# Optimization experiments

Hardware: AMD Instinct MI355X
Metric: run time of the kernel (lower is better)

The kernel has to match this reference:

```python
import jax, jax.numpy as jnp
import numpy as np

N_NODES = 50000
N_EDGES = 800000
IN_C = 128
OUT_C = 128
ALPHA = 0.2  # leaky_relu negative slope (args.egat_alpha)
EDGE_K = 3   # edgefeat width, fixed by W_out in-dim = 3*out_channels


def setup_inputs() -> dict:
    key = jax.random.key(0)
    k = jax.random.split(key, 7)
    h = jax.random.normal(k[0], (N_NODES, IN_C), dtype=jnp.float32)
    edge_index = jax.random.randint(k[1], (2, N_EDGES), 0, N_NODES, dtype=jnp.int64)
    edgefeat = jax.random.uniform(k[2], (N_EDGES, EDGE_K), dtype=jnp.float32)
    # glorot-initialized linear weights (stored as [in, out] for x @ W)
    def glorot(kk, fan_in, fan_out):
        lim = jnp.sqrt(6.0 / (fan_in + fan_out)).astype(jnp.float32)
        return jax.random.uniform(kk, (fan_in, fan_out), jnp.float32, -lim, lim)
    W = glorot(k[3], IN_C, OUT_C)
    a1 = glorot(k[4], OUT_C, 1)
    a2 = glorot(k[5], OUT_C, 1)
    W_out = glorot(k[6], EDGE_K * OUT_C, OUT_C)
    return {"h": h, "edge_index": edge_index, "edgefeat": edgefeat,
            "W": W, "a1": a1, "a2": a2, "W_out": W_out}


def reference(h, edge_index, edgefeat, W, a1, a2, W_out):
    src = edge_index[0]  # j: message source
    dst = edge_index[1]  # i: aggregation target
    n = h.shape[0]

    Wh = h @ W                                   # [N, C]
    s1 = Wh @ a1                                 # [N, 1] alpha_j scores
    s2 = Wh @ a2                                 # [N, 1] alpha_i scores

    # edge_update: leaky_relu(alpha_j + alpha_i) * edge_attr, then edge softmax over dst
    e = s1[src] + s2[dst]                        # [E, 1]
    e = jnp.where(e >= 0, e, ALPHA * e)
    alpha = e * edgefeat                         # [E, 3]
    m = jax.ops.segment_max(alpha, dst, num_segments=n)      # [N, 3]
    m = jnp.where(jnp.isfinite(m), m, 0.0)
    ex = jnp.exp(alpha - m[dst])
    denom = jax.ops.segment_sum(ex, dst, num_segments=n)     # [N, 3]
    att = ex / (denom[dst] + 1e-16)              # [E, 3] (dropout p applied at eval -> identity)

    # message: outer product att[E,3] x x_j[E,C] -> [E, 3C] -> W_out -> [E, C]
    x_j = Wh[src]                                # [E, C]
    msg = (att[:, :, None] * x_j[:, None, :]).reshape(att.shape[0], EDGE_K * Wh.shape[1])
    msg = msg @ W_out                            # [E, C]

    # aggregate: sum at destination nodes
    out = jax.ops.segment_sum(msg, dst, num_segments=n)      # [N, C]
    return out
```

## Files before the change

kernel.cpp:

```cpp
#include <hip/hip_runtime.h>
#include <hip/hip_bf16.h>

#define ALPHA 0.2f
typedef unsigned int uint32;
typedef __attribute__((ext_vector_type(8))) short short8;
typedef __attribute__((ext_vector_type(4))) float f32x4;

static __device__ __forceinline__ unsigned short f2bf(float f) {
    unsigned int u = __float_as_uint(f);
    u += 0x7fffu + ((u >> 16) & 1u);
    return (unsigned short)(u >> 16);
}
static __device__ __forceinline__ uint32 pk2bf(float lo, float hi) {
    return (uint32)f2bf(lo) | ((uint32)f2bf(hi) << 16);
}
static __device__ __forceinline__ float bflo(uint32 u) { return __uint_as_float(u << 16); }
static __device__ __forceinline__ float bfhi(uint32 u) { return __uint_as_float(u & 0xffff0000u); }

__global__ __launch_bounds__(256) void k1_hist_prep(const int* __restrict__ ei,
                                                    int* __restrict__ counts,
                                                    int* __restrict__ eslot, int E,
                                                    const float* __restrict__ W,
                                                    const float* __restrict__ Wout,
                                                    const float* __restrict__ a1,
                                                    const float* __restrict__ a2,
                                                    unsigned short* __restrict__ WBT,
                                                    unsigned short* __restrict__ WoutT,
                                                    float* __restrict__ w1f,
                                                    float* __restrict__ w2f, int nbh) {
    const int tid = threadIdx.x;
    if ((int)blockIdx.x < nbh) {
        int e = blockIdx.x * 256 + tid;
        if (e < E) eslot[e] = atomicAdd(&counts[ei[E + e]], 1);
        return;
    }
    int bp = blockIdx.x - nbh;
    if (bp < 8) {
        for (int n = bp * 16; n < bp * 16 + 16; ++n)
            for (int c = tid; c < 128; c += 256)
                WBT[n * 128 + c] = f2bf(W[c * 128 + n]);
    } else if (bp < 24) {
        int q = bp - 8;
        for (int n = q * 8; n < q * 8 + 8; ++n)
            for (int c = tid; c < 384; c += 256)
                WoutT[n * 384 + c] = f2bf(Wout[c * 128 + n]);
    } else {
        if (tid < 128) {
            float acc1 = 0.f, acc2 = 0.f;
            for (int c = 0; c < 128; ++c) {
                float w = W[tid * 128 + c];
                acc1 += w * a1[c];
                acc2 += w * a2[c];
            }
            w1f[tid] = acc1;
            w2f[tid] = acc2;
        }
    }
}

__global__ __launch_bounds__(256) void k2_mmy_scan(const float* __restrict__ h,
                                                   const unsigned short* __restrict__ WBT,
                                                   const float* __restrict__ w1f,
                                                   const float* __restrict__ w2f,
                                                   unsigned short* __restrict__ Whb,
                                                   float* __restrict__ s1,
                                                   uint2* __restrict__ PR, int M,
                                                   const int* __restrict__ counts,
                                                   int* __restrict__ rowptr,
                                                   int N, int E, int nbm) {
    __shared__ unsigned short As[64 * 128];
    __shared__ unsigned short Bs[128 * 128];
    __shared__ float ws1[128], ws2[128];
    __shared__ int wsums[4];
    __shared__ int base_s;
    const int tid = threadIdx.x;

    if ((int)blockIdx.x >= nbm) {
        const int bs   = blockIdx.x - nbm;
        const int lane = tid & 63, wv = tid >> 6;
        const int limit = bs * 1024;
        int acc = 0;
        for (int i = tid * 4; i < limit; i += 1024) {
            int4 v = *(const int4*)(counts + i);
            acc += v.x + v.y + v.z + v.w;
        }
#pragma unroll
        for (int off = 32; off > 0; off >>= 1) acc += __shfl_down(acc, off);
        if (lane == 0) wsums[wv] = acc;
        __syncthreads();
        if (tid == 0) base_s = wsums[0] + wsums[1] + wsums[2] + wsums[3];
        __syncthreads();
        int i0 = bs * 1024 + tid * 4;
        int v0 = 0, v1 = 0, v2 = 0, v3 = 0;
        if (i0 + 3 < N) {
            int4 v = *(const int4*)(counts + i0);
            v0 = v.x; v1 = v.y; v2 = v.z; v3 = v.w;
        } else {
            if (i0 + 0 < N) v0 = counts[i0 + 0];
            if (i0 + 1 < N) v1 = counts[i0 + 1];
            if (i0 + 2 < N) v2 = counts[i0 + 2];
            if (i0 + 3 < N) v3 = counts[i0 + 3];
        }
        int tt = v0 + v1 + v2 + v3;
        int incl = tt;
#pragma unroll
        for (int off = 1; off < 64; off <<= 1) {
            int t = __shfl_up(incl, off);
            if (lane >= off) incl += t;
        }
        __syncthreads();
        if (lane == 63) wsums[wv] = incl;
        __syncthreads();
        int woff = 0;
        for (int w2 = 0; w2 < wv; ++w2) woff += wsums[w2];
        int base = base_s + woff + (incl - tt);
        if (i0 + 0 < N) { rowptr[i0 + 0] = base;                PR[i0 + 0].y = (uint32)base; }
        if (i0 + 1 < N) { rowptr[i0 + 1] = base + v0;           PR[i0 + 1].y = (uint32)(base + v0); }
        if (i0 + 2 < N) { rowptr[i0 + 2] = base + v0 + v1;      PR[i0 + 2].y = (uint32)(base + v0 + v1); }
        if (i0 + 3 < N) { rowptr[i0 + 3] = base + v0 + v1 + v2; PR[i0 + 3].y = (uint32)(base + v0 + v1 + v2); }
        if (bs == 0 && tid == 0) rowptr[N] = E;
        return;
    }

    const int lane = tid & 63;
    const int w    = tid >> 6;
    const int row0 = blockIdx.x * 64;

    if (tid < 128) ws1[tid] = w1f[tid];
    else           ws2[tid - 128] = w2f[tid - 128];
    __syncthreads();

    const float4* h4 = (const float4*)h;
    float sp1[4], sp2[4];
#pragma unroll
    for (int m = 0; m < 4; ++m) { sp1[m] = 0.f; sp2[m] = 0.f; }
#pragma unroll
    for (int m = 0; m < 4; ++m) {
        int i = m * 256 + tid;
        int r = i >> 4, g = i & 15;
        int rg = row0 + r;
        float4 va = make_float4(0.f, 0.f, 0.f, 0.f), vb = va;
        if (rg < M) {
            va = h4[(size_t)rg * 32 + g * 2];
            vb = h4[(size_t)rg * 32 + g * 2 + 1];
        }
        float4 wa1 = *(const float4*)(ws1 + g * 8);
        float4 wb1 = *(const float4*)(ws1 + g * 8 + 4);
        float4 wa2 = *(const float4*)(ws2 + g * 8);
        float4 wb2 = *(const float4*)(ws2 + g * 8 + 4);
        sp1[m] += va.x * wa1.x + va.y * wa1.y + va.z * wa1.z + va.w * wa1.w
                + vb.x * wb1.x + vb.y * wb1.y + vb.z * wb1.z + vb.w * wb1.w;
        sp2[m] += va.x * wa2.x + va.y * wa2.y + va.z * wa2.z + va.w * wa2.w
                + vb.x * wb2.x + vb.y * wb2.y + vb.z * wb2.z + vb.w * wb2.w;
        uint4 u;
        u.x = pk2bf(va.x, va.y); u.y = pk2bf(va.z, va.w);
        u.z = pk2bf(vb.x, vb.y); u.w = pk2bf(vb.z, vb.w);
        *(uint4*)(As + r * 128 + ((g ^ (r & 15)) * 8)) = u;
    }
#pragma unroll
    for (int m = 0; m < 4; ++m) {
#pragma unroll
        for (int off = 1; off < 16; off <<= 1) {
            sp1[m] += __shfl_xor(sp1[m], off);
            sp2[m] += __shfl_xor(sp2[m], off);
        }
    }
    if ((tid & 15) == 0) {
#pragma unroll
        for (int m = 0; m < 4; ++m) {
            int rg = row0 + m * 16 + (tid >> 4);
            if (rg < M) { s1[rg] = sp1[m]; PR[rg].x = __float_as_uint(sp2[m]); }
        }
    }

#pragma unroll
    for (int m = 0; m < 8; ++m) {
        int i = m * 256 + tid;
        int n = i >> 4, g = i & 15;
        uint4 v = *(const uint4*)(WBT + n * 128 + g * 8);
        *(uint4*)(Bs + n * 128 + ((g ^ (n & 15)) * 8)) = v;
    }
    __syncthreads();

    const int ml   = lane & 15;
    const int quad = lane >> 4;
    f32x4 acc[8];
#pragma unroll
    for (int nt = 0; nt < 8; ++nt) acc[nt] = (f32x4){0.f, 0.f, 0.f, 0.f};
#pragma unroll
    for (int kc = 0; kc < 4; ++kc) {
        int gl = ((kc * 4 + quad) ^ ml) * 8;
        short8 af = *(const short8*)(As + (w * 16 + ml) * 128 + gl);
#pragma unroll
        for (int nt = 0; nt < 8; ++nt) {
            short8 bf = *(const short8*)(Bs + (nt * 16 + ml) * 128 + gl);
            acc[nt] = __builtin_amdgcn_mfma_f32_16x16x32_bf16(af, bf, acc[nt], 0, 0, 0);
        }
    }
    __syncthreads();
    unsigned short* Ct = Bs;
    int lrow = w * 16 + quad * 4;
#pragma unroll
    for (int r = 0; r < 4; ++r)
#pragma unroll
        for (int nt = 0; nt < 8; ++nt)
            Ct[(lrow + r) * 136 + nt * 16 + ml] = f2bf(acc[nt][r]);
    __syncthreads();
#pragma unroll
    for (int m = 0; m < 4; ++m) {
        int i = m * 256 + tid;
        int r2 = i >> 4, g = i & 15;
        int rg = row0 + r2;
        uint4 v = *(const uint4*)(Ct + r2 * 136 + g * 8);
        if (rg < M)
            *(uint4*)(Whb + (size_t)rg * 128 + g * 8) = v;
    }
}

__global__ __launch_bounds__(256) void scatter_kernel(const int* __restrict__ ei,
                                                      const float* __restrict__ ef,
                                                      const float* __restrict__ s1,
                                                      const uint2* __restrict__ PR,
                                                      const int* __restrict__ eslot,
                                                      uint2* __restrict__ rec8, int E) {
    int e = blockIdx.x * blockDim.x + threadIdx.x;
    if (e >= E) return;
    int src = ei[e];
    int dst = ei[E + e];
    uint2 pr = PR[dst];
    float s = s1[src] + __uint_as_float(pr.x);
    s = (s >= 0.f) ? s : ALPHA * s;
    unsigned short b0 = f2bf(__expf(s * ef[e * 3 + 0]));
    unsigned short b1 = f2bf(__expf(s * ef[e * 3 + 1]));
    unsigned short b2 = f2bf(__expf(s * ef[e * 3 + 2]));
    uint2 rv;
    rv.x = (uint32)src | ((uint32)(b0 & 0x7fffu) << 17);
    rv.y = (uint32)(b1 & 0x7fffu) | ((uint32)(b2 & 0x7fffu) << 15);
    int pos = (int)pr.y + eslot[e];
    rec8[pos] = rv;
}

__global__ __launch_bounds__(256) void agg_fused(const uint2* __restrict__ rec8,
                                                 const int* __restrict__ rowptr,
                                                 const uint32* __restrict__ Yu,
                                                 const unsigned short* __restrict__ WoutT,
                                                 float* __restrict__ out, int N) {
    __shared__ uint32 zs32[16 * 192];
    const int tid  = threadIdx.x;
    const int lane = tid & 63, w = tid >> 6;
    const int ml   = lane & 15, quad = lane >> 4;
    const int nb   = blockIdx.x * 16;

#pragma unroll
    for (int rnd = 0; rnd < 4; ++rnd) {
        int r    = rnd * 4 + w;
        int node = nb + r;
        if (node >= N) continue;
        int beg = rowptr[node], end = rowptr[node + 1];

        float d0 = 0.f, d1 = 0.f, d2 = 0.f;
        float z0l = 0.f, z0h = 0.f, z1l = 0.f, z1h = 0.f, z2l = 0.f, z2h = 0.f;
        int j = beg;
        for (; j + 7 < end; j += 8) {
            uint2 rr[8];
#pragma unroll
            for (int q = 0; q < 8; ++q) rr[q] = rec8[j + q];
            uint32 sx[8], sy[8];
#pragma unroll
            for (int q = 0; q < 8; ++q) {
                sx[q] = __builtin_amdgcn_readfirstlane(rr[q].x);
                sy[q] = __builtin_amdgcn_readfirstlane(rr[q].y);
            }
            uint32 u[8];
#pragma unroll
            for (int q = 0; q < 8; ++q)
                u[q] = Yu[(size_t)(sx[q] & 0x1ffffu) * 64 + lane];
#pragma unroll
            for (int q = 0; q < 8; ++q) {
                float w0 = __uint_as_float((sx[q] >> 1) & 0x7fff0000u);
                float w1 = __uint_as_float((sy[q] << 16) & 0x7fff0000u);
                float w2 = __uint_as_float((sy[q] << 1) & 0x7fff0000u);
                d0 += w0; d1 += w1; d2 += w2;
                float yl = bflo(u[q]), yh = bfhi(u[q]);
                z0l += w0 * yl; z0h += w0 * yh;
                z1l += w1 * yl; z1h += w1 * yh;
                z2l += w2 * yl; z2h += w2 * yh;
            }
        }
        for (; j + 3 < end; j += 4) {
            uint2 rr[4];
#pragma unroll
            for (int q = 0; q < 4; ++q) rr[q] = rec8[j + q];
            uint32 sx[4], sy[4];
#pragma unroll
            for (int q = 0; q < 4; ++q) {
                sx[q] = __builtin_amdgcn_readfirstlane(rr[q].x);
                sy[q] = __builtin_amdgcn_readfirstlane(rr[q].y);
            }
            uint32 u[4];
#pragma unroll
            for (int q = 0; q < 4; ++q)
                u[q] = Yu[(size_t)(sx[q] & 0x1ffffu) * 64 + lane];
#pragma unroll
            for (int q = 0; q < 4; ++q) {
                float w0 = __uint_as_float((sx[q] >> 1) & 0x7fff0000u);
                float w1 = __uint_as_float((sy[q] << 16) & 0x7fff0000u);
                float w2 = __uint_as_float((sy[q] << 1) & 0x7fff0000u);
                d0 += w0; d1 += w1; d2 += w2;
                float yl = bflo(u[q]), yh = bfhi(u[q]);
                z0l += w0 * yl; z0h += w0 * yh;
                z1l += w1 * yl; z1h += w1 * yh;
                z2l += w2 * yl; z2h += w2 * yh;
            }
        }
        for (; j < end; ++j) {
            uint2 r0 = rec8[j];
            uint32 sx = __builtin_amdgcn_readfirstlane(r0.x);
            uint32 sy = __builtin_amdgcn_readfirstlane(r0.y);
            uint32 u0 = Yu[(size_t)(sx & 0x1ffffu) * 64 + lane];
            float w0 = __uint_as_float((sx >> 1) & 0x7fff0000u);
            float w1 = __uint_as_float((sy << 16) & 0x7fff0000u);
            float w2 = __uint_as_float((sy << 1) & 0x7fff0000u);
            d0 += w0; d1 += w1; d2 += w2;
            float yl = bflo(u0), yh = bfhi(u0);
            z0l += w0 * yl; z0h += w0 * yh;
            z1l += w1 * yl; z1h += w1 * yh;
            z2l += w2 * yl; z2h += w2 * yh;
        }
        float i0 = 1.f / (d0 + 1e-16f);
        float i1 = 1.f / (d1 + 1e-16f);
        float i2 = 1.f / (d2 + 1e-16f);
        uint32 zp[3] = { pk2bf(z0l * i0, z0h * i0),
                         pk2bf(z1l * i1, z1h * i1),
                         pk2bf(z2l * i2, z2h * i2) };
#pragma unroll
        for (int k = 0; k < 3; ++k) {
            int g  = k * 16 + (lane >> 2);
            int sg = (g & ~7) | ((g ^ r) & 7);
            zs32[r * 192 + sg * 4 + (lane & 3)] = zp[k];
        }
    }
    __syncthreads();

    const int n0 = w * 32;
    f32x4 acc[2];
    acc[0] = (f32x4){0.f, 0.f, 0.f, 0.f};
    acc[1] = (f32x4){0.f, 0.f, 0.f, 0.f};
    const unsigned short* zs16 = (const unsigned short*)zs32;
#pragma unroll
    for (int ks = 0; ks < 12; ++ks) {
        int g  = ks * 4 + quad;
        int sg = (g & ~7) | ((g ^ ml) & 7);
        short8 af = *(const short8*)(zs16 + ml * 384 + sg * 8);
#pragma unroll
        for (int nt = 0; nt < 2; ++nt) {
            short8 bf = *(const short8*)(WoutT + (size_t)(n0 + nt * 16 + ml) * 384
                                         + ks * 32 + quad * 8);
            acc[nt] = __builtin_amdgcn_mfma_f32_16x16x32_bf16(af, bf, acc[nt], 0, 0, 0);
        }
    }
    __syncthreads();
    float* Ct = (float*)zs32;
#pragma unroll
    for (int r = 0; r < 4; ++r)
#pragma unroll
        for (int nt = 0; nt < 2; ++nt)
            Ct[(quad * 4 + r) * 132 + n0 + nt * 16 + ml] = acc[nt][r];
    __syncthreads();
#pragma unroll
    for (int m = 0; m < 2; ++m) {
        int i   = m * 256 + tid;
        int row = i >> 5, g = i & 31;
        int node = nb + row;
        if (node < N)
            *(float4*)(out + (size_t)node * 128 + g * 4) = *(const float4*)(Ct + row * 132 + g * 4);
    }
}

extern "C" void kernel_launch(void* const* d_in, const int* in_sizes, int n_in,
                              void* d_out, int out_size, void* d_ws, size_t ws_size,
                              hipStream_t stream) {
    const float* h    = (const float*)d_in[0];
    const int*   ei   = (const int*)d_in[1];
    const float* ef   = (const float*)d_in[2];
    const float* W    = (const float*)d_in[3];
    const float* a1   = (const float*)d_in[4];
    const float* a2   = (const float*)d_in[5];
    const float* Wout = (const float*)d_in[6];
    float*       out  = (float*)d_out;

    const int N = in_sizes[0] / 128;
    const int E = in_sizes[2] / 3;
    const int nchunk = (N + 1023) / 1024;
    const int nbh    = (E + 255) / 256;
    const int nbm    = (N + 63) / 64;

    uint2* rec8 = (uint2*)d_ws;
    unsigned short* Whb = (unsigned short*)(rec8 + E);
    unsigned short* WBT = Whb + (size_t)N * 128;
    unsigned short* WoutT = WBT + 128 * 128;
    float* w1f  = (float*)(WoutT + 128 * 384);
    float* w2f  = w1f + 128;
    float* s1   = w2f + 128;
    uint2* PR   = (uint2*)(s1 + N);
    int* rowptr = (int*)(PR + N);
    int* counts = rowptr + N + 4;
    int* eslot  = counts + N;

    (void)hipMemsetAsync(counts, 0, (size_t)N * sizeof(int), stream);

    k1_hist_prep<<<nbh + 25, 256, 0, stream>>>(ei, counts, eslot, E,
                                               W, Wout, a1, a2, WBT, WoutT, w1f, w2f, nbh);
    k2_mmy_scan<<<nbm + nchunk, 256, 0, stream>>>(h, WBT, w1f, w2f, Whb, s1, PR, N,
                                                  counts, rowptr, N, E, nbm);
    scatter_kernel<<<(E + 255) / 256, 256, 0, stream>>>(ei, ef, s1, PR, eslot, rec8, E);
    agg_fused<<<(N + 15) / 16, 256, 0, stream>>>(rec8, rowptr, (const uint32*)Whb,
                                                 WoutT, out, N);
}
```

Measured before the change: 234.8 us.

## Use 1024-thread blocks with one wave per node and split-K MFMA

The fused aggregation kernel now launches 1024 threads per block so each of 16 waves gathers one destination node, replacing four sequential rounds per wave. The W_out projection is split across K halves: 16 waves each compute one 16-column tile over half the K dimension, and the two partial results are summed from shared memory before the store. This aims to expose more memory-level parallelism in the irregular gather phase. In exchange it adds a larger shared buffer and an extra reduction pass, and large blocks may limit occupancy and scheduling flexibility.

```diff
diff --git a/kernel.cpp b/kernel.cpp
--- a/kernel.cpp
+++ b/kernel.cpp
@@ -240,22 +240,20 @@
     rec8[pos] = rv;
 }
 
-__global__ __launch_bounds__(256) void agg_fused(const uint2* __restrict__ rec8,
-                                                 const int* __restrict__ rowptr,
-                                                 const uint32* __restrict__ Yu,
-                                                 const unsigned short* __restrict__ WoutT,
-                                                 float* __restrict__ out, int N) {
-    __shared__ uint32 zs32[16 * 192];
+__global__ __launch_bounds__(1024) void agg_fused(const uint2* __restrict__ rec8,
+                                                  const int* __restrict__ rowptr,
+                                                  const uint32* __restrict__ Yu,
+                                                  const unsigned short* __restrict__ WoutT,
+                                                  float* __restrict__ out, int N) {
+    __shared__ float CtS[2 * 16 * 132];
+    uint32* zs32 = (uint32*)CtS;
     const int tid  = threadIdx.x;
     const int lane = tid & 63, w = tid >> 6;
     const int ml   = lane & 15, quad = lane >> 4;
     const int nb   = blockIdx.x * 16;
-
-#pragma unroll
-    for (int rnd = 0; rnd < 4; ++rnd) {
-        int r    = rnd * 4 + w;
-        int node = nb + r;
-        if (node >= N) continue;
+    const int node = nb + w;
+
+    if (node < N) {
         int beg = rowptr[node], end = rowptr[node + 1];
 
         float d0 = 0.f, d1 = 0.f, d2 = 0.f;
@@ -336,44 +334,42 @@
 #pragma unroll
         for (int k = 0; k < 3; ++k) {
             int g  = k * 16 + (lane >> 2);
-            int sg = (g & ~7) | ((g ^ r) & 7);
-            zs32[r * 192 + sg * 4 + (lane & 3)] = zp[k];
-        }
-    }
-    __syncthreads();
-
-    const int n0 = w * 32;
-    f32x4 acc[2];
-    acc[0] = (f32x4){0.f, 0.f, 0.f, 0.f};
-    acc[1] = (f32x4){0.f, 0.f, 0.f, 0.f};
+            int sg = (g & ~7) | ((g ^ w) & 7);
+            zs32[w * 192 + sg * 4 + (lane & 3)] = zp[k];
+        }
+    } else {
+#pragma unroll
+        for (int k = 0; k < 3; ++k)
+            zs32[w * 192 + k * 64 + lane] = 0u;
+    }
+    __syncthreads();
+
+    const int n0 = (w & 7) * 16;
+    const int kh = w >> 3;
+    f32x4 acc = (f32x4){0.f, 0.f, 0.f, 0.f};
     const unsigned short* zs16 = (const unsigned short*)zs32;
 #pragma unroll
-    for (int ks = 0; ks < 12; ++ks) {
-        int g  = ks * 4 + quad;
+    for (int ks = 0; ks < 6; ++ks) {
+        int g  = kh * 24 + ks * 4 + quad;
         int sg = (g & ~7) | ((g ^ ml) & 7);
         short8 af = *(const short8*)(zs16 + ml * 384 + sg * 8);
-#pragma unroll
-        for (int nt = 0; nt < 2; ++nt) {
-            short8 bf = *(const short8*)(WoutT + (size_t)(n0 + nt * 16 + ml) * 384
-                                         + ks * 32 + quad * 8);
-            acc[nt] = __builtin_amdgcn_mfma_f32_16x16x32_bf16(af, bf, acc[nt], 0, 0, 0);
-        }
-    }
-    __syncthreads();
-    float* Ct = (float*)zs32;
+        short8 bf = *(const short8*)(WoutT + (size_t)(n0 + ml) * 384 + g * 8);
+        acc = __builtin_amdgcn_mfma_f32_16x16x32_bf16(af, bf, acc, 0, 0, 0);
+    }
+    __syncthreads();
 #pragma unroll
     for (int r = 0; r < 4; ++r)
-#pragma unroll
-        for (int nt = 0; nt < 2; ++nt)
-            Ct[(quad * 4 + r) * 132 + n0 + nt * 16 + ml] = acc[nt][r];
-    __syncthreads();
-#pragma unroll
-    for (int m = 0; m < 2; ++m) {
-        int i   = m * 256 + tid;
-        int row = i >> 5, g = i & 31;
-        int node = nb + row;
-        if (node < N)
-            *(float4*)(out + (size_t)node * 128 + g * 4) = *(const float4*)(Ct + row * 132 + g * 4);
+        CtS[kh * 2112 + (quad * 4 + r) * 132 + n0 + ml] = acc[r];
+    __syncthreads();
+    if (tid < 512) {
+        int row = tid >> 5, g = tid & 31;
+        int nd  = nb + row;
+        if (nd < N) {
+            float4 a = *(const float4*)(CtS + row * 132 + g * 4);
+            float4 b = *(const float4*)(CtS + 2112 + row * 132 + g * 4);
+            *(float4*)(out + (size_t)nd * 128 + g * 4) =
+                make_float4(a.x + b.x, a.y + b.y, a.z + b.z, a.w + b.w);
+        }
     }
 }
 
@@ -414,6 +410,6 @@
     k2_mmy_scan<<<nbm + nchunk, 256, 0, stream>>>(h, WBT, w1f, w2f, Whb, s1, PR, N,
                                                   counts, rowptr, N, E, nbm);
     scatter_kernel<<<(E + 255) / 256, 256, 0, stream>>>(ei, ef, s1, PR, eslot, rec8, E);
-    agg_fused<<<(N + 15) / 16, 256, 0, stream>>>(rec8, rowptr, (const uint32*)Whb,
-                                                 WoutT, out, N);
-}
+    agg_fused<<<(N + 15) / 16, 1024, 0, stream>>>(rec8, rowptr, (const uint32*)Whb,
+                                                  WoutT, out, N);
+}
```

Result: no change. 238.1 us (+1.4%).
